# Kernel tuning notes

Hardware: AMD Instinct MI355X
Metric: run time of the kernel (lower is better)

## Reference

```python
import jax, jax.numpy as jnp
import numpy as np
import math

MAX_SIZE = 2048  # max_size init arg


def setup_inputs() -> dict:
    key = jax.random.key(0)
    k1, k2, k3 = jax.random.split(key, 3)
    B, S, D = 16, 1024, 512
    PRED = 256
    data = jax.random.normal(k1, (B, S, D), dtype=jnp.float32)
    W = jax.random.normal(k2, (PRED, D), dtype=jnp.float32) * (1.0 / math.sqrt(D))
    b = jax.random.normal(k3, (PRED,), dtype=jnp.float32) * 0.01
    return {"data": data, "W": W, "b": b}


def reference(data, W, b):
    # data: [B, S, D]; self-attention with q=k=v=data
    B, S, D = data.shape
    pred_len = W.shape[0]
    scale = 1.0 / math.sqrt(D)
    scores = jnp.einsum('bsd,btd->bst', data, data) * scale          # [B,S,S]
    prob = jax.nn.softmax(scores, axis=-1)
    attn = jnp.einsum('bst,btd->bsd', prob, data)                     # [B,S,D]
    # NOTE: the original concatenates a 'mask' block (rows S..2S) onto attn,
    # but the per-timestep Linear loop only reads rows 0..S-1, so the mask
    # never affects the output (dead code). The loop collapses to one GEMM.
    lin = jnp.einsum('bsd,pd->bsp', attn, W) + b                      # [B,S,pred_len]
    out = jnp.zeros((B, MAX_SIZE, pred_len), dtype=data.dtype)
    out = out.at[:, :S, :].set(lin)
    return out
```

## Files before the change

kernel.cpp:

```cpp
#include <hip/hip_runtime.h>
#include <cstdint>
#include <cstddef>

#define B_    16
#define S_    1024
#define D_    512
#define P_    256
#define MAXS_ 2048

typedef unsigned short u16;
typedef unsigned int   u32;
typedef _Float16 f16;
typedef _Float16 f16x8 __attribute__((ext_vector_type(8)));
typedef float  f32x4  __attribute__((ext_vector_type(4)));
typedef unsigned short u16x4 __attribute__((ext_vector_type(4)));
typedef unsigned short u16x8 __attribute__((ext_vector_type(8)));

__device__ __forceinline__ void gld_lds16(const void* g, void* l) {
  __builtin_amdgcn_global_load_lds(
      (const __attribute__((address_space(1))) u32*)g,
      (__attribute__((address_space(3))) u32*)l, 16, 0, 0);
}

__device__ __forceinline__ u16 f2h(float f) {
  return __builtin_bit_cast(u16, (f16)f);
}
__device__ __forceinline__ float h2f(u16 h) {
  return (float)__builtin_bit_cast(f16, h);
}

__global__ void convert_f16_kernel(const float* __restrict__ src, u16* __restrict__ dst, long n4) {
  long stride = (long)gridDim.x * blockDim.x;
  for (long i = (long)blockIdx.x * blockDim.x + threadIdx.x; i < n4; i += stride) {
    float4 v = ((const float4*)src)[i];
    u16x4 o;
    o[0] = f2h(v.x); o[1] = f2h(v.y); o[2] = f2h(v.z); o[3] = f2h(v.w);
    ((u16x4*)dst)[i] = o;
  }
}

__global__ __launch_bounds__(512, 2) void qk_pipe(
    const u16* __restrict__ A, u16* __restrict__ Cout, float scale) {
  extern __shared__ __align__(16) char smem[];
  const int tid  = threadIdx.x;
  const int lane = tid & 63;
  const int w    = tid >> 6;
  const int wm   = w >> 2;
  const int wn   = w & 3;
  const int lr   = lane & 15;
  const int hi   = lane >> 4;

  const int bz = blockIdx.z;
  const int I0 = blockIdx.y * 256;
  const int J0 = blockIdx.x * 256;
  const u16* Ab = A + (long)bz * (S_ * D_);

  auto stageP = [&](int s, int part) {
    if (s >= 16) return;
    char* dst = smem + (s & 3) * 32768 + part * 16384;
    const int base = part ? J0 : I0;
    const int k0 = s * 32;
    #pragma unroll
    for (int i = 0; i < 2; ++i) {
      int cid   = i * 512 + tid;
      int inner = cid >> 2;
      int c     = (cid & 3) ^ ((inner >> 1) & 3);
      gld_lds16(Ab + (size_t)(base + inner) * D_ + k0 + c * 8, dst + cid * 16);
    }
  };

  f32x4 acc[8][4] = {};

  stageP(0, 0); stageP(0, 1);
  stageP(1, 0); stageP(1, 1);
  stageP(2, 0); stageP(2, 1);
  asm volatile("s_waitcnt vmcnt(8)" ::: "memory");
  __builtin_amdgcn_s_barrier();

  for (int s = 0; s < 16; ++s) {
    const char* sl = smem + (s & 3) * 32768;
    f16x8 bf[4];
    {
      f16x8 af[4];
      #pragma unroll
      for (int mq = 0; mq < 4; ++mq) {
        int row = wm * 128 + mq * 16 + lr;
        int cp  = hi ^ ((row >> 1) & 3);
        af[mq] = *(const f16x8*)(sl + row * 64 + cp * 16);
      }
      #pragma unroll
      for (int n = 0; n < 4; ++n) {
        int row = wn * 64 + n * 16 + lr;
        int cp  = hi ^ ((row >> 1) & 3);
        bf[n] = *(const f16x8*)(sl + 16384 + row * 64 + cp * 16);
      }
      stageP(s + 3, 0);
      __builtin_amdgcn_s_barrier();
      asm volatile("s_waitcnt lgkmcnt(0)" ::: "memory");
      __builtin_amdgcn_sched_barrier(0);
      __builtin_amdgcn_s_setprio(1);
      #pragma unroll
      for (int mq = 0; mq < 4; ++mq)
        #pragma unroll
        for (int n = 0; n < 4; ++n)
          acc[mq][n] = __builtin_amdgcn_mfma_f32_16x16x32_f16(af[mq], bf[n], acc[mq][n], 0, 0, 0);
      __builtin_amdgcn_s_setprio(0);
      __builtin_amdgcn_s_barrier();
    }
    {
      f16x8 af[4];
      #pragma unroll
      for (int mq = 0; mq < 4; ++mq) {
        int row = wm * 128 + 64 + mq * 16 + lr;
        int cp  = hi ^ ((row >> 1) & 3);
        af[mq] = *(const f16x8*)(sl + row * 64 + cp * 16);
      }
      stageP(s + 3, 1);
      __builtin_amdgcn_s_barrier();
      asm volatile("s_waitcnt lgkmcnt(0)" ::: "memory");
      __builtin_amdgcn_sched_barrier(0);
      __builtin_amdgcn_s_setprio(1);
      #pragma unroll
      for (int mq = 0; mq < 4; ++mq)
        #pragma unroll
        for (int n = 0; n < 4; ++n)
          acc[4 + mq][n] = __builtin_amdgcn_mfma_f32_16x16x32_f16(af[mq], bf[n], acc[4 + mq][n], 0, 0, 0);
      __builtin_amdgcn_s_setprio(0);
      if (s <= 12)      asm volatile("s_waitcnt vmcnt(8)" ::: "memory");
      else if (s == 13) asm volatile("s_waitcnt vmcnt(4)" ::: "memory");
      else if (s == 14) asm volatile("s_waitcnt vmcnt(0)" ::: "memory");
      __builtin_amdgcn_s_barrier();
    }
  }

  u16* Cb = Cout + (long)bz * S_ * S_;
  const int row0 = I0 + wm * 128;
  const int col0 = J0 + wn * 64;
  #pragma unroll
  for (int m = 0; m < 8; ++m) {
    #pragma unroll
    for (int i = 0; i < 4; ++i) {
      int r = row0 + m * 16 + (hi << 2) + i;
      #pragma unroll
      for (int n = 0; n < 4; ++n) {
        int c = col0 + n * 16 + lr;
        Cb[(size_t)r * S_ + c] = f2h(acc[m][n][i] * scale);
      }
    }
  }
}

__global__ __launch_bounds__(512, 4) void smpv_kernel(
    const u16* __restrict__ scores, const u16* __restrict__ VWT,
    float* __restrict__ out, const float* __restrict__ bias) {
  extern __shared__ __align__(16) char smem[];
  constexpr int SZB = 8192 + 32768;
  const int tid  = threadIdx.x;
  const int lane = tid & 63;
  const int w    = tid >> 6;
  const int bz   = blockIdx.z;
  const int yt   = blockIdx.y;

  float* ob = out + (long)bz * MAXS_ * P_;
  if (yt >= 16) {
    float4* o = (float4*)(ob + (size_t)yt * 64 * P_);
    for (int i = tid; i < 64 * P_ / 4; i += 512)
      o[i] = make_float4(0.f, 0.f, 0.f, 0.f);
    return;
  }

  const int q0 = yt * 64;
  const u16* sb = scores + ((long)bz * S_ + q0) * S_;
  const float l2e = 1.4426950408889634f;

  float* smStat = (float*)smem;
  {
    const u16* rp = sb + (size_t)(w * 8) * S_ + lane * 16;
    for (int j = 0; j < 8; ++j) {
      u16x8 a0 = *(const u16x8*)(rp + (size_t)j * S_);
      u16x8 a1 = *(const u16x8*)(rp + (size_t)j * S_ + 8);
      float v[16];
      #pragma unroll
      for (int k = 0; k < 8; ++k) { v[k] = h2f(a0[k]); v[8 + k] = h2f(a1[k]); }
      float mx = v[0];
      #pragma unroll
      for (int k = 1; k < 16; ++k) mx = fmaxf(mx, v[k]);
      #pragma unroll
      for (int off = 32; off > 0; off >>= 1) mx = fmaxf(mx, __shfl_xor(mx, off));
      float sum = 0.f;
      #pragma unroll
      for (int k = 0; k < 16; ++k) sum += exp2f((v[k] - mx) * l2e);
      #pragma unroll
      for (int off = 32; off > 0; off >>= 1) sum += __shfl_xor(sum, off);
      if (lane == 0) {
        smStat[(w * 8 + j) * 2]     = mx;
        smStat[(w * 8 + j) * 2 + 1] = 1.f / sum;
      }
    }
  }
  __syncthreads();
  const int   arow = tid >> 3;
  const float am   = smStat[arow * 2];
  const float ail  = smStat[arow * 2 + 1];
  __syncthreads();

  const int wm = w >> 2, wn = w & 3;
  const u16* Vb = VWT + (long)bz * P_ * S_;
  const int ac8 = tid & 7;

  auto stageB = [&](int buf, int k0) {
    char* dB = smem + buf * SZB + 8192;
    #pragma unroll
    for (int i = 0; i < 4; ++i) {
      int cid = i * 512 + tid;
      int row = cid >> 3;
      int c   = (cid & 7) ^ (row & 7);
      gld_lds16(Vb + (size_t)row * S_ + k0 + c * 8, dB + cid * 16);
    }
  };
  auto writeA = [&](int buf, u16x8 raw) {
    u16x8 pv;
    #pragma unroll
    for (int j = 0; j < 8; ++j)
      pv[j] = f2h(exp2f((h2f(raw[j]) - am) * l2e) * ail);
    int c = ac8 ^ (arow & 7);
    *(u16x8*)(smem + buf * SZB + (arow * 8 + c) * 16) = pv;
  };

  f32x4 acc[2][4] = {};

  {
    u16x8 a0 = *(const u16x8*)(sb + (size_t)arow * S_ + ac8 * 8);
    __builtin_amdgcn_sched_barrier(0);
    stageB(0, 0);
    __builtin_amdgcn_sched_barrier(0);
    asm volatile("s_waitcnt vmcnt(4)" ::: "memory");
    writeA(0, a0);
    asm volatile("s_waitcnt vmcnt(0) lgkmcnt(0)" ::: "memory");
    __builtin_amdgcn_s_barrier();
  }

  for (int t = 0; t < 16; ++t) {
    const int cur = t & 1;
    const char* lA = smem + cur * SZB;
    const char* lB = lA + 8192;

    u16x8 anx;
    if (t < 15) {
      anx = *(const u16x8*)(sb + (size_t)arow * S_ + (t + 1) * 64 + ac8 * 8);
      __builtin_amdgcn_sched_barrier(0);
      stageB(cur ^ 1, (t + 1) * 64);
      __builtin_amdgcn_sched_barrier(0);
    }

    #pragma unroll
    for (int kk = 0; kk < 2; ++kk) {
      f16x8 af[2], bfv[4];
      #pragma unroll
      for (int m = 0; m < 2; ++m) {
        int row = wm * 32 + m * 16 + (lane & 15);
        int cp  = (kk * 4 + (lane >> 4)) ^ (row & 7);
        af[m] = *(const f16x8*)(lA + ((row * 8 + cp) << 4));
      }
      #pragma unroll
      for (int n = 0; n < 4; ++n) {
        int row = wn * 64 + n * 16 + (lane & 15);
        int cp  = (kk * 4 + (lane >> 4)) ^ (row & 7);
        bfv[n] = *(const f16x8*)(lB + ((row * 8 + cp) << 4));
      }
      __builtin_amdgcn_s_setprio(1);
      #pragma unroll
      for (int m = 0; m < 2; ++m)
        #pragma unroll
        for (int n = 0; n < 4; ++n)
          acc[m][n] = __builtin_amdgcn_mfma_f32_16x16x32_f16(af[m], bfv[n], acc[m][n], 0, 0, 0);
      __builtin_amdgcn_s_setprio(0);
    }

    if (t < 15) {
      asm volatile("s_waitcnt vmcnt(4)" ::: "memory");
      writeA(cur ^ 1, anx);
      asm volatile("s_waitcnt vmcnt(0) lgkmcnt(0)" ::: "memory");
      __builtin_amdgcn_s_barrier();
    }
  }

  const int lr = lane & 15, hi = lane >> 4;
  const int row0 = q0 + wm * 32;
  const int col0 = wn * 64;
  float bv[4];
  #pragma unroll
  for (int n = 0; n < 4; ++n) bv[n] = bias[col0 + n * 16 + lr];
  #pragma unroll
  for (int m = 0; m < 2; ++m) {
    #pragma unroll
    for (int i = 0; i < 4; ++i) {
      int r = row0 + m * 16 + (hi << 2) + i;
      #pragma unroll
      for (int n = 0; n < 4; ++n)
        ob[(size_t)r * P_ + col0 + n * 16 + lr] = acc[m][n][i] + bv[n];
    }
  }
}

template<int KK, int BM, int BN, int NW, int WNS>
__global__ __launch_bounds__(NW * 64, 1) void gemm_nt_small(
    const u16* __restrict__ A, const u16* __restrict__ Bm,
    u16* __restrict__ C, long sAb, long sBb, long sCb, int LDC) {
  constexpr int T   = NW * 64;
  constexpr int WMS = NW / WNS;
  constexpr int MF  = BM / (WMS * 16);
  constexpr int NF  = BN / (WNS * 16);
  constexpr int LA  = BM * 8 / T;
  constexpr int LB  = BN * 8 / T;
  constexpr int SZ  = (BM + BN) * 128;
  constexpr int NT  = KK / 64;

  extern __shared__ __align__(16) char smem[];
  const int tid  = threadIdx.x;
  const int lane = tid & 63;
  const int w    = tid >> 6;
  const int wm   = w / WNS;
  const int wn   = w % WNS;
  const int lr   = lane & 15;
  const int hi   = lane >> 4;

  const int bz = blockIdx.z;
  const int I0 = blockIdx.y * BM;
  const int J0 = blockIdx.x * BN;
  const u16* Ab = A  + (long)bz * sAb;
  const u16* Bb = Bm + (long)bz * sBb;

  auto stage = [&](int buf, int k0) {
    char* sA = smem + buf * SZ;
    char* sB = sA + BM * 128;
    #pragma unroll
    for (int i = 0; i < LA; ++i) {
      int cid = i * T + tid;
      int row = cid >> 3;
      int c   = (cid & 7) ^ (row & 7);
      gld_lds16(Ab + (size_t)(I0 + row) * KK + k0 + c * 8, sA + cid * 16);
    }
    #pragma unroll
    for (int i = 0; i < LB; ++i) {
      int cid = i * T + tid;
      int row = cid >> 3;
      int c   = (cid & 7) ^ (row & 7);
      gld_lds16(Bb + (size_t)(J0 + row) * KK + k0 + c * 8, sB + cid * 16);
    }
  };

  f32x4 acc[MF][NF] = {};
  stage(0, 0);
  for (int t = 0; t < NT; ++t) {
    const char* lA = smem + (t & 1) * SZ;
    const char* lB = lA + BM * 128;
    if (t + 1 < NT) {
      stage((t + 1) & 1, (t + 1) * 64);
      asm volatile("s_waitcnt vmcnt(%0)" :: "i"(LA + LB) : "memory");
    } else {
      asm volatile("s_waitcnt vmcnt(0)" ::: "memory");
    }
    __builtin_amdgcn_s_barrier();
    __builtin_amdgcn_sched_barrier(0);
    #pragma unroll
    for (int kk = 0; kk < 2; ++kk) {
      f16x8 af[MF], bfv[NF];
      #pragma unroll
      for (int m = 0; m < MF; ++m) {
        int row = wm * (MF * 16) + m * 16 + lr;
        int cp  = (kk * 4 + hi) ^ (row & 7);
        af[m] = *(const f16x8*)(lA + ((row * 8 + cp) << 4));
      }
      #pragma unroll
      for (int n = 0; n < NF; ++n) {
        int row = wn * (NF * 16) + n * 16 + lr;
        int cp  = (kk * 4 + hi) ^ (row & 7);
        bfv[n] = *(const f16x8*)(lB + ((row * 8 + cp) << 4));
      }
      __builtin_amdgcn_s_setprio(1);
      #pragma unroll
      for (int m = 0; m < MF; ++m)
        #pragma unroll
        for (int n = 0; n < NF; ++n)
          acc[m][n] = __builtin_amdgcn_mfma_f32_16x16x32_f16(af[m], bfv[n], acc[m][n], 0, 0, 0);
      __builtin_amdgcn_s_setprio(0);
    }
    __builtin_amdgcn_sched_barrier(0);
    __builtin_amdgcn_s_barrier();
  }

  const int row0 = I0 + wm * (MF * 16);
  const int col0 = J0 + wn * (NF * 16);
  #pragma unroll
  for (int m = 0; m < MF; ++m)
    #pragma unroll
    for (int i = 0; i < 4; ++i) {
      int r = row0 + m * 16 + (hi << 2) + i;
      #pragma unroll
      for (int n = 0; n < NF; ++n)
        C[(long)bz * sCb + (size_t)r * LDC + col0 + n * 16 + lr] = f2h(acc[m][n][i]);
    }
}

extern "C" void kernel_launch(void* const* d_in, const int* in_sizes, int n_in,
                              void* d_out, int out_size, void* d_ws, size_t ws_size,
                              hipStream_t stream) {
  const float* data = (const float*)d_in[0];
  const float* W    = (const float*)d_in[1];
  const float* bias = (const float*)d_in[2];
  float* out = (float*)d_out;
  char*  ws  = (char*)d_ws;

  const size_t MB = 1024 * 1024;
  u16* dataH   = (u16*)(ws);
  u16* Wh      = (u16*)(ws + 16 * MB);
  u16* scoresH = (u16*)(ws + 17 * MB);
  u16* VWT     = (u16*)(ws + 49 * MB);

  const float scale = 0.04419417382415922f;

  constexpr int SMEM_QK   = 4 * 32768;
  constexpr int SMEM_SMPV = 2 * (8192 + 32768);
  constexpr int SMEM_VW   = 2 * (64 + 256) * 128;

  (void)hipFuncSetAttribute((const void*)&qk_pipe,
                      hipFuncAttributeMaxDynamicSharedMemorySize, SMEM_QK);
  (void)hipFuncSetAttribute((const void*)&smpv_kernel,
                      hipFuncAttributeMaxDynamicSharedMemorySize, SMEM_SMPV);
  (void)hipFuncSetAttribute((const void*)&gemm_nt_small<512, 64, 256, 2, 2>,
                      hipFuncAttributeMaxDynamicSharedMemorySize, SMEM_VW);

  convert_f16_kernel<<<2048, 256, 0, stream>>>(data, dataH, (long)B_ * S_ * D_ / 4);
  convert_f16_kernel<<<64, 256, 0, stream>>>(W, Wh, (long)P_ * D_ / 4);

  gemm_nt_small<512, 64, 256, 2, 2><<<dim3(4, 4, 16), 128, SMEM_VW, stream>>>(
      Wh, dataH, VWT, 0L, (long)S_ * D_, (long)P_ * S_, S_);

  qk_pipe<<<dim3(4, 4, 16), 512, SMEM_QK, stream>>>(dataH, scoresH, scale);

  smpv_kernel<<<dim3(1, 32, 16), 512, SMEM_SMPV, stream>>>(
      scoresH, VWT, out, bias);
}
```

Measured before the change: 94.29 us.

## Split softmax row statistics into separate kernel and reshape PV tiling

Moves the per-row max and sum-of-exponentials computation out of the fused softmax·V kernel into a standalone stats kernel that writes (max, 1/sum) pairs to workspace. The PV kernel now uses 256 threads with four waves, each covering all 64 rows and a 64-column slice, and each thread stages two 8-element A chunks per step. This removes the serial stats prologue from the PV kernel but adds a kernel launch and an extra full read of the scores matrix. It also changes wait counts to vmcnt(0), which may reduce overlap between loads and compute.

```diff
diff --git a/kernel.cpp b/kernel.cpp
--- a/kernel.cpp
+++ b/kernel.cpp
@@ -150,115 +150,121 @@
   }
 }
 
-__global__ __launch_bounds__(512, 4) void smpv_kernel(
+__global__ __launch_bounds__(256) void stats_kernel(
+    const u16* __restrict__ scores, float2* __restrict__ rowstat) {
+  const int lane = threadIdx.x & 63;
+  const int wv   = threadIdx.x >> 6;
+  const long row = (long)blockIdx.x * 4 + wv;
+  const u16* src = scores + row * S_;
+
+  u16x8 a0 = *(const u16x8*)&src[lane * 16];
+  u16x8 a1 = *(const u16x8*)&src[lane * 16 + 8];
+  float v[16];
+  #pragma unroll
+  for (int j = 0; j < 8; ++j) { v[j] = h2f(a0[j]); v[8 + j] = h2f(a1[j]); }
+
+  float mx = v[0];
+  #pragma unroll
+  for (int j = 1; j < 16; ++j) mx = fmaxf(mx, v[j]);
+  #pragma unroll
+  for (int off = 32; off > 0; off >>= 1)
+    mx = fmaxf(mx, __shfl_xor(mx, off));
+
+  const float l2e = 1.4426950408889634f;
+  float sum = 0.f;
+  #pragma unroll
+  for (int j = 0; j < 16; ++j) sum += exp2f((v[j] - mx) * l2e);
+  #pragma unroll
+  for (int off = 32; off > 0; off >>= 1)
+    sum += __shfl_xor(sum, off);
+
+  if (lane == 0) rowstat[row] = make_float2(mx, 1.f / sum);
+}
+
+__global__ __launch_bounds__(256, 2) void pv_kernel(
     const u16* __restrict__ scores, const u16* __restrict__ VWT,
+    const float2* __restrict__ rowstat,
     float* __restrict__ out, const float* __restrict__ bias) {
   extern __shared__ __align__(16) char smem[];
-  constexpr int SZB = 8192 + 32768;
   const int tid  = threadIdx.x;
   const int lane = tid & 63;
-  const int w    = tid >> 6;
-  const int bz   = blockIdx.z;
-  const int yt   = blockIdx.y;
+  const int wn   = tid >> 6;
+  const int bz = blockIdx.z;
+  const int yt = blockIdx.y;
 
   float* ob = out + (long)bz * MAXS_ * P_;
   if (yt >= 16) {
     float4* o = (float4*)(ob + (size_t)yt * 64 * P_);
-    for (int i = tid; i < 64 * P_ / 4; i += 512)
+    for (int i = tid; i < 64 * P_ / 4; i += 256)
       o[i] = make_float4(0.f, 0.f, 0.f, 0.f);
     return;
   }
 
   const int q0 = yt * 64;
   const u16* sb = scores + ((long)bz * S_ + q0) * S_;
+  const u16* Vb = VWT + (long)bz * P_ * S_;
+
+  const int arow = tid >> 2;
+  const int ac   = tid & 3;
+  float2 st = rowstat[(long)bz * S_ + q0 + arow];
+  const float am = st.x, ail = st.y;
   const float l2e = 1.4426950408889634f;
 
-  float* smStat = (float*)smem;
-  {
-    const u16* rp = sb + (size_t)(w * 8) * S_ + lane * 16;
-    for (int j = 0; j < 8; ++j) {
-      u16x8 a0 = *(const u16x8*)(rp + (size_t)j * S_);
-      u16x8 a1 = *(const u16x8*)(rp + (size_t)j * S_ + 8);
-      float v[16];
-      #pragma unroll
-      for (int k = 0; k < 8; ++k) { v[k] = h2f(a0[k]); v[8 + k] = h2f(a1[k]); }
-      float mx = v[0];
-      #pragma unroll
-      for (int k = 1; k < 16; ++k) mx = fmaxf(mx, v[k]);
-      #pragma unroll
-      for (int off = 32; off > 0; off >>= 1) mx = fmaxf(mx, __shfl_xor(mx, off));
-      float sum = 0.f;
-      #pragma unroll
-      for (int k = 0; k < 16; ++k) sum += exp2f((v[k] - mx) * l2e);
-      #pragma unroll
-      for (int off = 32; off > 0; off >>= 1) sum += __shfl_xor(sum, off);
-      if (lane == 0) {
-        smStat[(w * 8 + j) * 2]     = mx;
-        smStat[(w * 8 + j) * 2 + 1] = 1.f / sum;
-      }
-    }
-  }
-  __syncthreads();
-  const int   arow = tid >> 3;
-  const float am   = smStat[arow * 2];
-  const float ail  = smStat[arow * 2 + 1];
-  __syncthreads();
-
-  const int wm = w >> 2, wn = w & 3;
-  const u16* Vb = VWT + (long)bz * P_ * S_;
-  const int ac8 = tid & 7;
-
-  auto stageB = [&](int buf, int k0) {
-    char* dB = smem + buf * SZB + 8192;
-    #pragma unroll
-    for (int i = 0; i < 4; ++i) {
-      int cid = i * 512 + tid;
+  auto stageB = [&](int t) {
+    char* dB = smem + 16384 + (t & 1) * 32768;
+    const int k0 = t * 64;
+    #pragma unroll
+    for (int i = 0; i < 8; ++i) {
+      int cid = i * 256 + tid;
       int row = cid >> 3;
       int c   = (cid & 7) ^ (row & 7);
       gld_lds16(Vb + (size_t)row * S_ + k0 + c * 8, dB + cid * 16);
     }
   };
-  auto writeA = [&](int buf, u16x8 raw) {
-    u16x8 pv;
-    #pragma unroll
-    for (int j = 0; j < 8; ++j)
-      pv[j] = f2h(exp2f((h2f(raw[j]) - am) * l2e) * ail);
-    int c = ac8 ^ (arow & 7);
-    *(u16x8*)(smem + buf * SZB + (arow * 8 + c) * 16) = pv;
+  auto writeA = [&](int buf, u16x8 r0, u16x8 r1) {
+    u16x8 p0, p1;
+    #pragma unroll
+    for (int j = 0; j < 8; ++j) {
+      p0[j] = f2h(exp2f((h2f(r0[j]) - am) * l2e) * ail);
+      p1[j] = f2h(exp2f((h2f(r1[j]) - am) * l2e) * ail);
+    }
+    int c0 = (ac * 2)     ^ (arow & 7);
+    int c1 = (ac * 2 + 1) ^ (arow & 7);
+    *(u16x8*)(smem + buf * 8192 + (arow * 8 + c0) * 16) = p0;
+    *(u16x8*)(smem + buf * 8192 + (arow * 8 + c1) * 16) = p1;
   };
 
-  f32x4 acc[2][4] = {};
-
-  {
-    u16x8 a0 = *(const u16x8*)(sb + (size_t)arow * S_ + ac8 * 8);
-    __builtin_amdgcn_sched_barrier(0);
-    stageB(0, 0);
-    __builtin_amdgcn_sched_barrier(0);
-    asm volatile("s_waitcnt vmcnt(4)" ::: "memory");
-    writeA(0, a0);
-    asm volatile("s_waitcnt vmcnt(0) lgkmcnt(0)" ::: "memory");
-    __builtin_amdgcn_s_barrier();
-  }
+  f32x4 acc[4][4] = {};
+  u16x8 a0, a1;
+
+  a0 = *(const u16x8*)(sb + (size_t)arow * S_ + ac * 16);
+  a1 = *(const u16x8*)(sb + (size_t)arow * S_ + ac * 16 + 8);
+  __builtin_amdgcn_sched_barrier(0);
+  stageB(0);
+  __builtin_amdgcn_sched_barrier(0);
+  asm volatile("s_waitcnt vmcnt(0)" ::: "memory");
+  writeA(0, a0, a1);
+  asm volatile("s_waitcnt lgkmcnt(0)" ::: "memory");
+  __builtin_amdgcn_s_barrier();
 
   for (int t = 0; t < 16; ++t) {
-    const int cur = t & 1;
-    const char* lA = smem + cur * SZB;
-    const char* lB = lA + 8192;
-
-    u16x8 anx;
+    const char* lA = smem + (t & 1) * 8192;
+    const char* lB = smem + 16384 + (t & 1) * 32768;
+
     if (t < 15) {
-      anx = *(const u16x8*)(sb + (size_t)arow * S_ + (t + 1) * 64 + ac8 * 8);
+      a0 = *(const u16x8*)(sb + (size_t)arow * S_ + (t + 1) * 64 + ac * 16);
+      a1 = *(const u16x8*)(sb + (size_t)arow * S_ + (t + 1) * 64 + ac * 16 + 8);
       __builtin_amdgcn_sched_barrier(0);
-      stageB(cur ^ 1, (t + 1) * 64);
+      stageB(t + 1);
       __builtin_amdgcn_sched_barrier(0);
     }
 
     #pragma unroll
     for (int kk = 0; kk < 2; ++kk) {
-      f16x8 af[2], bfv[4];
-      #pragma unroll
-      for (int m = 0; m < 2; ++m) {
-        int row = wm * 32 + m * 16 + (lane & 15);
+      f16x8 af[4], bf[4];
+      #pragma unroll
+      for (int m = 0; m < 4; ++m) {
+        int row = m * 16 + (lane & 15);
         int cp  = (kk * 4 + (lane >> 4)) ^ (row & 7);
         af[m] = *(const f16x8*)(lA + ((row * 8 + cp) << 4));
       }
@@ -266,36 +272,35 @@
       for (int n = 0; n < 4; ++n) {
         int row = wn * 64 + n * 16 + (lane & 15);
         int cp  = (kk * 4 + (lane >> 4)) ^ (row & 7);
-        bfv[n] = *(const f16x8*)(lB + ((row * 8 + cp) << 4));
+        bf[n] = *(const f16x8*)(lB + ((row * 8 + cp) << 4));
       }
       __builtin_amdgcn_s_setprio(1);
       #pragma unroll
-      for (int m = 0; m < 2; ++m)
+      for (int m = 0; m < 4; ++m)
         #pragma unroll
         for (int n = 0; n < 4; ++n)
-          acc[m][n] = __builtin_amdgcn_mfma_f32_16x16x32_f16(af[m], bfv[n], acc[m][n], 0, 0, 0);
+          acc[m][n] = __builtin_amdgcn_mfma_f32_16x16x32_f16(af[m], bf[n], acc[m][n], 0, 0, 0);
       __builtin_amdgcn_s_setprio(0);
     }
 
     if (t < 15) {
-      asm volatile("s_waitcnt vmcnt(4)" ::: "memory");
-      writeA(cur ^ 1, anx);
-      asm volatile("s_waitcnt vmcnt(0) lgkmcnt(0)" ::: "memory");
+      asm volatile("s_waitcnt vmcnt(0)" ::: "memory");
+      writeA((t + 1) & 1, a0, a1);
+      asm volatile("s_waitcnt lgkmcnt(0)" ::: "memory");
       __builtin_amdgcn_s_barrier();
     }
   }
 
   const int lr = lane & 15, hi = lane >> 4;
-  const int row0 = q0 + wm * 32;
   const int col0 = wn * 64;
   float bv[4];
   #pragma unroll
   for (int n = 0; n < 4; ++n) bv[n] = bias[col0 + n * 16 + lr];
   #pragma unroll
-  for (int m = 0; m < 2; ++m) {
+  for (int m = 0; m < 4; ++m) {
     #pragma unroll
     for (int i = 0; i < 4; ++i) {
-      int r = row0 + m * 16 + (hi << 2) + i;
+      int r = q0 + m * 16 + (hi << 2) + i;
       #pragma unroll
       for (int n = 0; n < 4; ++n)
         ob[(size_t)r * P_ + col0 + n * 16 + lr] = acc[m][n][i] + bv[n];
@@ -413,21 +418,22 @@
   char*  ws  = (char*)d_ws;
 
   const size_t MB = 1024 * 1024;
-  u16* dataH   = (u16*)(ws);
-  u16* Wh      = (u16*)(ws + 16 * MB);
-  u16* scoresH = (u16*)(ws + 17 * MB);
-  u16* VWT     = (u16*)(ws + 49 * MB);
+  u16*    dataH   = (u16*)(ws);
+  u16*    Wh      = (u16*)(ws + 16 * MB);
+  u16*    scoresH = (u16*)(ws + 17 * MB);
+  u16*    VWT     = (u16*)(ws + 49 * MB);
+  float2* rowstat = (float2*)(ws + 57 * MB);
 
   const float scale = 0.04419417382415922f;
 
-  constexpr int SMEM_QK   = 4 * 32768;
-  constexpr int SMEM_SMPV = 2 * (8192 + 32768);
-  constexpr int SMEM_VW   = 2 * (64 + 256) * 128;
+  constexpr int SMEM_QK = 4 * 32768;
+  constexpr int SMEM_PV = 2 * 8192 + 2 * 32768;
+  constexpr int SMEM_VW = 2 * (64 + 256) * 128;
 
   (void)hipFuncSetAttribute((const void*)&qk_pipe,
                       hipFuncAttributeMaxDynamicSharedMemorySize, SMEM_QK);
-  (void)hipFuncSetAttribute((const void*)&smpv_kernel,
-                      hipFuncAttributeMaxDynamicSharedMemorySize, SMEM_SMPV);
+  (void)hipFuncSetAttribute((const void*)&pv_kernel,
+                      hipFuncAttributeMaxDynamicSharedMemorySize, SMEM_PV);
   (void)hipFuncSetAttribute((const void*)&gemm_nt_small<512, 64, 256, 2, 2>,
                       hipFuncAttributeMaxDynamicSharedMemorySize, SMEM_VW);
 
@@ -439,6 +445,8 @@
 
   qk_pipe<<<dim3(4, 4, 16), 512, SMEM_QK, stream>>>(dataH, scoresH, scale);
 
-  smpv_kernel<<<dim3(1, 32, 16), 512, SMEM_SMPV, stream>>>(
-      scoresH, VWT, out, bias);
-}
+  stats_kernel<<<4096, 256, 0, stream>>>(scoresH, rowstat);
+
+  pv_kernel<<<dim3(1, 32, 16), 256, SMEM_PV, stream>>>(
+      scoresH, VWT, rowstat, out, bias);
+}
```

Measured after the change: 91.37 us. -3.1%, faster.
